# Optimization experiments

Measured on AMD Instinct MI355X. Metric: run time of the kernel, lower is better.

Reference implementation:

```python
import jax, jax.numpy as jnp
import numpy as np

N_NODES = 100000
N_EDGES = 1600000
N_GRAPHS = 512


def gcn_conv(x, src, dst, W, b, num_nodes):
    """PyG GCNConv: add self-loops, sym-normalize, aggregate, add bias."""
    xw = x @ W  # [N, out]
    # degree over destination nodes, +1 for the implicit self-loop
    deg = jax.ops.segment_sum(jnp.ones(src.shape[0], xw.dtype), dst,
                              num_segments=num_nodes) + 1.0
    dinv = jax.lax.rsqrt(deg)  # deg >= 1, safe
    norm = dinv[src] * dinv[dst]  # [E]
    agg = jax.ops.segment_sum(xw[src] * norm[:, None], dst,
                              num_segments=num_nodes)
    # self-loop contribution: dinv[i]^2 * xw[i]
    agg = agg + xw * (dinv * dinv)[:, None]
    return agg + b


def global_mean_pool(x, batch, num_graphs):
    sums = jax.ops.segment_sum(x, batch, num_segments=num_graphs)
    cnts = jax.ops.segment_sum(jnp.ones(x.shape[0], x.dtype), batch,
                               num_segments=num_graphs)
    return sums / jnp.maximum(cnts, 1.0)[:, None]


def setup_inputs() -> dict:
    key = jax.random.key(0)
    ks = jax.random.split(key, 9)
    x = jax.random.normal(ks[0], (N_NODES, 3), dtype=jnp.float32)
    edge_index = jax.random.randint(ks[1], (2, N_EDGES), 0, N_NODES, dtype=jnp.int64)
    batch = jnp.sort(jax.random.randint(ks[2], (N_NODES,), 0, N_GRAPHS, dtype=jnp.int64))
    W1 = jax.random.normal(ks[3], (3, 32), dtype=jnp.float32) * 0.5
    b1 = jax.random.normal(ks[4], (32,), dtype=jnp.float32) * 0.1
    W2 = jax.random.normal(ks[5], (32, 32), dtype=jnp.float32) * 0.2
    b2 = jax.random.normal(ks[6], (32,), dtype=jnp.float32) * 0.1
    Wl = jax.random.normal(ks[7], (32, 2), dtype=jnp.float32) * 0.2
    bl = jax.random.normal(ks[8], (2,), dtype=jnp.float32) * 0.1
    return {"x": x, "edge_index": edge_index, "batch": batch,
            "W1": W1, "b1": b1, "W2": W2, "b2": b2, "Wl": Wl, "bl": bl}


def reference(x, edge_index, batch, W1, b1, W2, b2, Wl, bl):
    src, dst = edge_index[0], edge_index[1]
    h = jax.nn.relu(gcn_conv(x, src, dst, W1, b1, N_NODES))
    h = jax.nn.relu(gcn_conv(h, src, dst, W2, b2, N_NODES))
    g = global_mean_pool(h, batch, N_GRAPHS)  # [G, 32]
    return g @ Wl + bl  # [G, 2]
```

## Files before the change

### kernel.cpp

```cpp
#include <hip/hip_runtime.h>
#include <hip/hip_fp16.h>

#define NN 100000
#define NE 1600000
#define NG 512
#define F  32

#define BSH    8
#define BNODES 256
#define NB     ((NN + BNODES - 1) / BNODES)
#define CAP    5120
#define PCHUNK 4096
#define EPT    8
#define NWGP   ((NE + PCHUNK - 1) / PCHUNK)

__global__ void k_partition(const int* __restrict__ src, const int* __restrict__ dst,
                            int* __restrict__ cursor, int* __restrict__ part) {
    __shared__ int   s_cnt[NB];
    __shared__ int   s_lstart[NB];
    __shared__ int   s_base[NB];
    __shared__ int   wsum[8];
    __shared__ int   lsort[PCHUNK];
    __shared__ short lbkt[PCHUNK];
    int tid = threadIdx.x;
    for (int i = tid; i < NB; i += 512) s_cnt[i] = 0;
    __syncthreads();
    int e0 = blockIdx.x * PCHUNK;
    int e1 = min(e0 + PCHUNK, NE);
    int pk[EPT]; short bk[EPT];
    int m = 0;
#pragma unroll
    for (int k = 0; k < EPT; ++k) {
        int e = e0 + tid + k * 512;
        if (e < e1) {
            int d = dst[e];
            pk[m] = (src[e] << 8) | (d & (BNODES - 1));
            bk[m] = (short)(d >> BSH);
            atomicAdd(&s_cnt[bk[m]], 1);
            ++m;
        }
    }
    __syncthreads();
    int cv = (tid < NB) ? s_cnt[tid] : 0;
    int v = cv;
#pragma unroll
    for (int o = 1; o < 64; o <<= 1) {
        int t = __shfl_up(v, o, 64);
        if ((tid & 63) >= o) v += t;
    }
    if ((tid & 63) == 63) wsum[tid >> 6] = v;
    __syncthreads();
    int add = 0;
    for (int w = 0; w < (tid >> 6); ++w) add += wsum[w];
    int excl = v + add - cv;
    if (tid < NB) {
        s_lstart[tid] = excl;
        if (cv) s_base[tid] = tid * CAP + atomicAdd(&cursor[tid], cv);
        s_cnt[tid] = 0;
    }
    __syncthreads();
    for (int k = 0; k < m; ++k) {
        int b = bk[k];
        int r = s_lstart[b] + atomicAdd(&s_cnt[b], 1);
        lsort[r] = pk[k];
        lbkt[r]  = (short)b;
    }
    __syncthreads();
    int cnt = e1 - e0;
    for (int i = tid; i < cnt; i += 512) {
        int b = lbkt[i];
        part[s_base[b] + (i - s_lstart[b])] = lsort[i];
    }
}

__global__ void k_fill2a(const int* __restrict__ part, const int* __restrict__ cursor,
                         const float* __restrict__ x,
                         int* __restrict__ rowpack, float* __restrict__ dinv,
                         float4* __restrict__ xd) {
    __shared__ int cnt[BNODES];
    __shared__ int wsum[4];
    int b = blockIdx.x, tid = threadIdx.x;
    int node0 = b << BSH;
    int s0 = b * CAP, s1 = s0 + cursor[b];
    cnt[tid] = 0;
    __syncthreads();
    for (int i = s0 + tid; i < s1; i += 256) atomicAdd(&cnt[part[i] & (BNODES - 1)], 1);
    __syncthreads();
    int c = cnt[tid];
    int v = c;
#pragma unroll
    for (int o = 1; o < 64; o <<= 1) {
        int t = __shfl_up(v, o, 64);
        if ((tid & 63) >= o) v += t;
    }
    if ((tid & 63) == 63) wsum[tid >> 6] = v;
    __syncthreads();
    int add = 0;
    for (int w = 0; w < (tid >> 6); ++w) add += wsum[w];
    int excl = v + add - c;
    int n = node0 + tid;
    if (n < NN) {
        rowpack[n] = ((s0 + excl) << 10) | c;
        float d = rsqrtf((float)c + 1.0f);
        dinv[n] = d;
        xd[n] = make_float4(d * x[n * 3 + 0], d * x[n * 3 + 1], d * x[n * 3 + 2], d);
    }
}

__global__ void k_fill2b(const int* __restrict__ part, const int* __restrict__ cursor,
                         const int* __restrict__ rowpack, const float4* __restrict__ xd,
                         const float* __restrict__ W1, const float* __restrict__ b1,
                         int* __restrict__ csr, __half2* __restrict__ g1) {
    __shared__ int lcsr[CAP];
    __shared__ int off[BNODES];
    __shared__ float W1s[3 * F];
    __shared__ float b1s[F];
    int b = blockIdx.x, tid = threadIdx.x;
    int node0 = b << BSH;
    int s0 = b * CAP;
    int cnt = cursor[b];
    if (tid < 3 * F) W1s[tid] = W1[tid];
    if (tid < F) b1s[tid] = b1[tid];
    int n = node0 + tid;
    int pack = (n < NN) ? rowpack[n] : (s0 << 10);
    off[tid] = (pack >> 10) - s0;
    __syncthreads();
    for (int i = tid; i < cnt; i += 256) {
        int p = part[s0 + i];
        int pos = atomicAdd(&off[p & (BNODES - 1)], 1);
        lcsr[pos] = p >> 8;
    }
    __syncthreads();
    for (int i = tid; i < cnt; i += 256) csr[s0 + i] = lcsr[i];
    if (n < NN) {
        int deg = pack & 1023;
        int beg = (pack >> 10) - s0;
        int end = beg + deg;
        float ax = 0.0f, ay = 0.0f, az = 0.0f;
        int e = beg;
        for (; e + 7 < end; e += 8) {
#pragma unroll
            for (int u = 0; u < 8; ++u) {
                float4 v = xd[lcsr[e + u]];
                ax += v.x; ay += v.y; az += v.z;
            }
        }
        for (; e < end; ++e) {
            float4 v = xd[lcsr[e]];
            ax += v.x; ay += v.y; az += v.z;
        }
        float4 sf = xd[n];
        float dn = sf.w;
        float cx = dn * (ax + sf.x), cy = dn * (ay + sf.y), cz = dn * (az + sf.z);
        __half2 tmp[16];
#pragma unroll
        for (int j = 0; j < 16; ++j) {
            int f0 = 2 * j, f1 = 2 * j + 1;
            float v0 = cx * W1s[f0] + cy * W1s[F + f0] + cz * W1s[2 * F + f0] + b1s[f0];
            float v1 = cx * W1s[f1] + cy * W1s[F + f1] + cz * W1s[2 * F + f1] + b1s[f1];
            tmp[j] = __floats2half2_rn(dn * fmaxf(v0, 0.0f), dn * fmaxf(v1, 0.0f));
        }
        uint4* hv = (uint4*)(g1 + (size_t)n * 16);
        const uint4* tv = (const uint4*)tmp;
        hv[0] = tv[0]; hv[1] = tv[1]; hv[2] = tv[2]; hv[3] = tv[3];
    }
}

__global__ void k_gather2p(const int* __restrict__ rowpack, const int* __restrict__ csr,
                           const __half2* __restrict__ g1, const float* __restrict__ dinv,
                           const int* __restrict__ batch,
                           const float* __restrict__ W2, const float* __restrict__ b2,
                           float* __restrict__ gsum) {
    __shared__ float W2s[F * F];
    __shared__ float b2s[F];
    __shared__ float ts[16][F];
    __shared__ float hs[16][F];
    __shared__ int bat[16];
    int tid = threadIdx.x;
    int nb = blockIdx.x * 16;
    for (int i = tid; i < F * F; i += 256) W2s[i] = W2[i];
    if (tid < F) b2s[tid] = b2[tid];
    if (tid < 16) bat[tid] = batch[nb + tid];
    int nl = tid >> 4, j = tid & 15;
    int n = nb + nl;
    {
        int pack = rowpack[n];
        int beg = pack >> 10, end = beg + (pack & 1023);
        float ax = 0.0f, ay = 0.0f;
        int e = beg;
        for (; e + 7 < end; e += 8) {
            int s0 = csr[e],     s1 = csr[e + 1], s2 = csr[e + 2], s3 = csr[e + 3];
            int s4 = csr[e + 4], s5 = csr[e + 5], s6 = csr[e + 6], s7 = csr[e + 7];
            float2 v0 = __half22float2(g1[s0 * 16 + j]);
            float2 v1 = __half22float2(g1[s1 * 16 + j]);
            float2 v2 = __half22float2(g1[s2 * 16 + j]);
            float2 v3 = __half22float2(g1[s3 * 16 + j]);
            float2 v4 = __half22float2(g1[s4 * 16 + j]);
            float2 v5 = __half22float2(g1[s5 * 16 + j]);
            float2 v6 = __half22float2(g1[s6 * 16 + j]);
            float2 v7 = __half22float2(g1[s7 * 16 + j]);
            ax += ((v0.x + v1.x) + (v2.x + v3.x)) + ((v4.x + v5.x) + (v6.x + v7.x));
            ay += ((v0.y + v1.y) + (v2.y + v3.y)) + ((v4.y + v5.y) + (v6.y + v7.y));
        }
        for (; e + 3 < end; e += 4) {
            int s0 = csr[e], s1 = csr[e + 1], s2 = csr[e + 2], s3 = csr[e + 3];
            float2 v0 = __half22float2(g1[s0 * 16 + j]);
            float2 v1 = __half22float2(g1[s1 * 16 + j]);
            float2 v2 = __half22float2(g1[s2 * 16 + j]);
            float2 v3 = __half22float2(g1[s3 * 16 + j]);
            ax += (v0.x + v1.x) + (v2.x + v3.x);
            ay += (v0.y + v1.y) + (v2.y + v3.y);
        }
        for (; e < end; ++e) {
            float2 v = __half22float2(g1[csr[e] * 16 + j]);
            ax += v.x; ay += v.y;
        }
        float dn = dinv[n];
        float2 sf = __half22float2(g1[n * 16 + j]);
        ts[nl][2 * j]     = dn * (ax + sf.x);
        ts[nl][2 * j + 1] = dn * (ay + sf.y);
    }
    __syncthreads();
    {
        int f = tid & 31;
        int nn0 = tid >> 5;
#pragma unroll
        for (int pass = 0; pass < 2; ++pass) {
            int nn = nn0 + pass * 8;
            float acc = b2s[f];
#pragma unroll
            for (int k = 0; k < F; ++k) acc += ts[nn][k] * W2s[k * F + f];
            hs[nn][f] = fmaxf(acc, 0.0f);
        }
    }
    __syncthreads();
    if (tid < F) {
        int g0 = bat[0], gmax = bat[15];
        for (int g = g0; g <= gmax; ++g) {
            float s = 0.0f;
#pragma unroll
            for (int i = 0; i < 16; ++i) if (bat[i] == g) s += hs[i][tid];
            atomicAdd(&gsum[g * F + tid], s);
        }
    }
}

__global__ void k_head(const float* __restrict__ gsum, const int* __restrict__ batch,
                       const float* __restrict__ Wl, const float* __restrict__ bl,
                       float* __restrict__ out) {
    int g = blockIdx.x * blockDim.x + threadIdx.x;
    if (g >= NG) return;
    int lo = 0, hi = NN;
    while (lo < hi) { int m = (lo + hi) >> 1; if (batch[m] < g) lo = m + 1; else hi = m; }
    int s = lo;
    lo = 0; hi = NN;
    while (lo < hi) { int m = (lo + hi) >> 1; if (batch[m] < g + 1) lo = m + 1; else hi = m; }
    float inv = 1.0f / fmaxf((float)(lo - s), 1.0f);
    float a0 = 0.0f, a1 = 0.0f;
#pragma unroll
    for (int k = 0; k < F; ++k) {
        float m = gsum[g * F + k] * inv;
        a0 += m * Wl[k * 2 + 0];
        a1 += m * Wl[k * 2 + 1];
    }
    out[g * 2 + 0] = a0 + bl[0];
    out[g * 2 + 1] = a1 + bl[1];
}

extern "C" void kernel_launch(void* const* d_in, const int* in_sizes, int n_in,
                              void* d_out, int out_size, void* d_ws, size_t ws_size,
                              hipStream_t stream) {
    const float* x     = (const float*)d_in[0];
    const int*   eidx  = (const int*)d_in[1];
    const int*   batch = (const int*)d_in[2];
    const float* W1    = (const float*)d_in[3];
    const float* b1    = (const float*)d_in[4];
    const float* W2    = (const float*)d_in[5];
    const float* b2    = (const float*)d_in[6];
    const float* Wl    = (const float*)d_in[7];
    const float* bl    = (const float*)d_in[8];
    float*       out   = (float*)d_out;

    const int* src = eidx;
    const int* dst = eidx + NE;

    char* base = (char*)d_ws;
    size_t off = 0;
    auto alloc = [&](size_t bytes) {
        void* p = base + off;
        off = (off + bytes + 127) & ~(size_t)127;
        return p;
    };
    int*     cursor  = (int*)alloc(NB * sizeof(int) + (size_t)NG * F * sizeof(float));
    float*   gsum    = (float*)(cursor + NB);
    int*     rowpack = (int*)alloc(NN * sizeof(int));
    int*     part    = (int*)alloc((size_t)NB * CAP * sizeof(int));
    int*     csr     = (int*)alloc((size_t)NB * CAP * sizeof(int));
    float*   dinv    = (float*)alloc(NN * sizeof(float));
    float4*  xd      = (float4*)alloc(NN * sizeof(float4));
    __half2* g1      = (__half2*)alloc((size_t)NN * 16 * sizeof(__half2));

    const int B = 256;
    const int gG16 = NN / 16;

    hipMemsetAsync(cursor, 0, NB * sizeof(int) + (size_t)NG * F * sizeof(float), stream);

    k_partition<<<NWGP, 512, 0, stream>>>(src, dst, cursor, part);
    k_fill2a   <<<NB,   B,   0, stream>>>(part, cursor, x, rowpack, dinv, xd);
    k_fill2b   <<<NB,   B,   0, stream>>>(part, cursor, rowpack, xd, W1, b1, csr, g1);

    k_gather2p<<<gG16, B, 0, stream>>>(rowpack, csr, g1, dinv, batch, W2, b2, gsum);

    k_head<<<(NG + B - 1) / B, B, 0, stream>>>(gsum, batch, Wl, bl, out);
}
```

Measured before the change: 166.4 us.

## Fuse head into gather, use 4 threads per node with 16-byte loads

The layer-2 gather now gives each node 4 threads that each load a uint4 (8 halfs), where it used to give 16 threads that each load a half2. This cuts load instruction count and raises bytes per request. Each block handles 64 nodes. The final linear head is folded into the gather epilogue: per-graph partial sums are projected by Wl, reduced with shuffles, scaled by precomputed inverse counts and atomically added to the output. Inverse counts and bias initialisation move into block 0 of fill2a. This removes the k_head launch and the gsum memset, but adds float-atomic ordering nondeterminism and a serial binary-search tail in one block.

```diff
diff --git a/kernel.cpp b/kernel.cpp
--- a/kernel.cpp
+++ b/kernel.cpp
@@ -74,9 +74,11 @@
 }
 
 __global__ void k_fill2a(const int* __restrict__ part, const int* __restrict__ cursor,
-                         const float* __restrict__ x,
+                         const float* __restrict__ x, const int* __restrict__ batch,
+                         const float* __restrict__ bl,
                          int* __restrict__ rowpack, float* __restrict__ dinv,
-                         float4* __restrict__ xd) {
+                         float4* __restrict__ xd, float* __restrict__ inv_cnt,
+                         float* __restrict__ out) {
     __shared__ int cnt[BNODES];
     __shared__ int wsum[4];
     int b = blockIdx.x, tid = threadIdx.x;
@@ -104,6 +106,20 @@
         float d = rsqrtf((float)c + 1.0f);
         dinv[n] = d;
         xd[n] = make_float4(d * x[n * 3 + 0], d * x[n * 3 + 1], d * x[n * 3 + 2], d);
+    }
+    if (b == 0) {
+        float bl0 = bl[0], bl1 = bl[1];
+#pragma unroll
+        for (int g = tid; g < NG; g += 256) {
+            int lo = 0, hi = NN;
+            while (lo < hi) { int m = (lo + hi) >> 1; if (batch[m] < g) lo = m + 1; else hi = m; }
+            int s = lo;
+            lo = 0; hi = NN;
+            while (lo < hi) { int m = (lo + hi) >> 1; if (batch[m] < g + 1) lo = m + 1; else hi = m; }
+            inv_cnt[g] = 1.0f / fmaxf((float)(lo - s), 1.0f);
+            out[g * 2 + 0] = bl0;
+            out[g * 2 + 1] = bl1;
+        }
     }
 }
 
@@ -170,101 +186,92 @@
                            const __half2* __restrict__ g1, const float* __restrict__ dinv,
                            const int* __restrict__ batch,
                            const float* __restrict__ W2, const float* __restrict__ b2,
-                           float* __restrict__ gsum) {
+                           const float* __restrict__ Wl, const float* __restrict__ inv_cnt,
+                           float* __restrict__ out) {
     __shared__ float W2s[F * F];
     __shared__ float b2s[F];
-    __shared__ float ts[16][F];
-    __shared__ float hs[16][F];
-    __shared__ int bat[16];
+    __shared__ float Wls[F * 2];
+    __shared__ float ts[64][F];
+    __shared__ float hs[64][F];
+    __shared__ int bat[64];
     int tid = threadIdx.x;
-    int nb = blockIdx.x * 16;
+    int nb = blockIdx.x * 64;
     for (int i = tid; i < F * F; i += 256) W2s[i] = W2[i];
     if (tid < F) b2s[tid] = b2[tid];
-    if (tid < 16) bat[tid] = batch[nb + tid];
-    int nl = tid >> 4, j = tid & 15;
-    int n = nb + nl;
-    {
+    if (tid < 2 * F) Wls[tid] = Wl[tid];
+    if (tid < 64) bat[tid] = (nb + tid < NN) ? batch[nb + tid] : -1;
+    int nl = tid >> 2;
+    int j  = tid & 3;
+    int n  = nb + nl;
+    if (n < NN) {
+        const uint4* gp = (const uint4*)g1;
         int pack = rowpack[n];
         int beg = pack >> 10, end = beg + (pack & 1023);
-        float ax = 0.0f, ay = 0.0f;
+        float a0 = 0, a1 = 0, a2 = 0, a3 = 0, a4 = 0, a5 = 0, a6 = 0, a7 = 0;
         int e = beg;
-        for (; e + 7 < end; e += 8) {
-            int s0 = csr[e],     s1 = csr[e + 1], s2 = csr[e + 2], s3 = csr[e + 3];
-            int s4 = csr[e + 4], s5 = csr[e + 5], s6 = csr[e + 6], s7 = csr[e + 7];
-            float2 v0 = __half22float2(g1[s0 * 16 + j]);
-            float2 v1 = __half22float2(g1[s1 * 16 + j]);
-            float2 v2 = __half22float2(g1[s2 * 16 + j]);
-            float2 v3 = __half22float2(g1[s3 * 16 + j]);
-            float2 v4 = __half22float2(g1[s4 * 16 + j]);
-            float2 v5 = __half22float2(g1[s5 * 16 + j]);
-            float2 v6 = __half22float2(g1[s6 * 16 + j]);
-            float2 v7 = __half22float2(g1[s7 * 16 + j]);
-            ax += ((v0.x + v1.x) + (v2.x + v3.x)) + ((v4.x + v5.x) + (v6.x + v7.x));
-            ay += ((v0.y + v1.y) + (v2.y + v3.y)) + ((v4.y + v5.y) + (v6.y + v7.y));
-        }
         for (; e + 3 < end; e += 4) {
             int s0 = csr[e], s1 = csr[e + 1], s2 = csr[e + 2], s3 = csr[e + 3];
-            float2 v0 = __half22float2(g1[s0 * 16 + j]);
-            float2 v1 = __half22float2(g1[s1 * 16 + j]);
-            float2 v2 = __half22float2(g1[s2 * 16 + j]);
-            float2 v3 = __half22float2(g1[s3 * 16 + j]);
-            ax += (v0.x + v1.x) + (v2.x + v3.x);
-            ay += (v0.y + v1.y) + (v2.y + v3.y);
+            uint4 u0 = gp[s0 * 4 + j];
+            uint4 u1 = gp[s1 * 4 + j];
+            uint4 u2 = gp[s2 * 4 + j];
+            uint4 u3 = gp[s3 * 4 + j];
+#define ACC8(u) { \
+            float2 t0 = __half22float2(*(const __half2*)&u.x); \
+            float2 t1 = __half22float2(*(const __half2*)&u.y); \
+            float2 t2 = __half22float2(*(const __half2*)&u.z); \
+            float2 t3 = __half22float2(*(const __half2*)&u.w); \
+            a0 += t0.x; a1 += t0.y; a2 += t1.x; a3 += t1.y; \
+            a4 += t2.x; a5 += t2.y; a6 += t3.x; a7 += t3.y; }
+            ACC8(u0) ACC8(u1) ACC8(u2) ACC8(u3)
         }
         for (; e < end; ++e) {
-            float2 v = __half22float2(g1[csr[e] * 16 + j]);
-            ax += v.x; ay += v.y;
-        }
+            int s = csr[e];
+            uint4 u = gp[s * 4 + j];
+            ACC8(u)
+        }
+        uint4 su = gp[n * 4 + j];
+        ACC8(su)
+#undef ACC8
         float dn = dinv[n];
-        float2 sf = __half22float2(g1[n * 16 + j]);
-        ts[nl][2 * j]     = dn * (ax + sf.x);
-        ts[nl][2 * j + 1] = dn * (ay + sf.y);
+        float* tr = &ts[nl][8 * j];
+        tr[0] = dn * a0; tr[1] = dn * a1; tr[2] = dn * a2; tr[3] = dn * a3;
+        tr[4] = dn * a4; tr[5] = dn * a5; tr[6] = dn * a6; tr[7] = dn * a7;
     }
     __syncthreads();
     {
         int f = tid & 31;
-        int nn0 = tid >> 5;
-#pragma unroll
-        for (int pass = 0; pass < 2; ++pass) {
-            int nn = nn0 + pass * 8;
+        int r = tid >> 5;
+#pragma unroll
+        for (int pass = 0; pass < 8; ++pass) {
+            int nn = r + pass * 8;
             float acc = b2s[f];
 #pragma unroll
             for (int k = 0; k < F; ++k) acc += ts[nn][k] * W2s[k * F + f];
-            hs[nn][f] = fmaxf(acc, 0.0f);
+            hs[nn][f] = (nb + nn < NN) ? fmaxf(acc, 0.0f) : 0.0f;
         }
     }
     __syncthreads();
     if (tid < F) {
-        int g0 = bat[0], gmax = bat[15];
+        int last = min(63, NN - 1 - nb);
+        int g0 = bat[0], gmax = bat[last];
+        float w0 = Wls[2 * tid], w1 = Wls[2 * tid + 1];
         for (int g = g0; g <= gmax; ++g) {
             float s = 0.0f;
 #pragma unroll
-            for (int i = 0; i < 16; ++i) if (bat[i] == g) s += hs[i][tid];
-            atomicAdd(&gsum[g * F + tid], s);
-        }
-    }
-}
-
-__global__ void k_head(const float* __restrict__ gsum, const int* __restrict__ batch,
-                       const float* __restrict__ Wl, const float* __restrict__ bl,
-                       float* __restrict__ out) {
-    int g = blockIdx.x * blockDim.x + threadIdx.x;
-    if (g >= NG) return;
-    int lo = 0, hi = NN;
-    while (lo < hi) { int m = (lo + hi) >> 1; if (batch[m] < g) lo = m + 1; else hi = m; }
-    int s = lo;
-    lo = 0; hi = NN;
-    while (lo < hi) { int m = (lo + hi) >> 1; if (batch[m] < g + 1) lo = m + 1; else hi = m; }
-    float inv = 1.0f / fmaxf((float)(lo - s), 1.0f);
-    float a0 = 0.0f, a1 = 0.0f;
-#pragma unroll
-    for (int k = 0; k < F; ++k) {
-        float m = gsum[g * F + k] * inv;
-        a0 += m * Wl[k * 2 + 0];
-        a1 += m * Wl[k * 2 + 1];
-    }
-    out[g * 2 + 0] = a0 + bl[0];
-    out[g * 2 + 1] = a1 + bl[1];
+            for (int i = 0; i < 64; ++i) if (bat[i] == g) s += hs[i][tid];
+            float p0 = s * w0, p1 = s * w1;
+#pragma unroll
+            for (int o = 16; o >= 1; o >>= 1) {
+                p0 += __shfl_xor(p0, o, 32);
+                p1 += __shfl_xor(p1, o, 32);
+            }
+            if (tid == 0) {
+                float ic = inv_cnt[g];
+                atomicAdd(&out[g * 2 + 0], p0 * ic);
+                atomicAdd(&out[g * 2 + 1], p1 * ic);
+            }
+        }
+    }
 }
 
 extern "C" void kernel_launch(void* const* d_in, const int* in_sizes, int n_in,
@@ -291,8 +298,8 @@
         off = (off + bytes + 127) & ~(size_t)127;
         return p;
     };
-    int*     cursor  = (int*)alloc(NB * sizeof(int) + (size_t)NG * F * sizeof(float));
-    float*   gsum    = (float*)(cursor + NB);
+    int*     cursor  = (int*)alloc(NB * sizeof(int));
+    float*   inv_cnt = (float*)alloc(NG * sizeof(float));
     int*     rowpack = (int*)alloc(NN * sizeof(int));
     int*     part    = (int*)alloc((size_t)NB * CAP * sizeof(int));
     int*     csr     = (int*)alloc((size_t)NB * CAP * sizeof(int));
@@ -301,15 +308,15 @@
     __half2* g1      = (__half2*)alloc((size_t)NN * 16 * sizeof(__half2));
 
     const int B = 256;
-    const int gG16 = NN / 16;
-
-    hipMemsetAsync(cursor, 0, NB * sizeof(int) + (size_t)NG * F * sizeof(float), stream);
+    const int gG64 = (NN + 63) / 64;
+
+    hipMemsetAsync(cursor, 0, NB * sizeof(int), stream);
 
     k_partition<<<NWGP, 512, 0, stream>>>(src, dst, cursor, part);
-    k_fill2a   <<<NB,   B,   0, stream>>>(part, cursor, x, rowpack, dinv, xd);
+    k_fill2a   <<<NB,   B,   0, stream>>>(part, cursor, x, batch, bl,
+                                          rowpack, dinv, xd, inv_cnt, out);
     k_fill2b   <<<NB,   B,   0, stream>>>(part, cursor, rowpack, xd, W1, b1, csr, g1);
 
-    k_gather2p<<<gG16, B, 0, stream>>>(rowpack, csr, g1, dinv, batch, W2, b2, gsum);
-
-    k_head<<<(NG + B - 1) / B, B, 0, stream>>>(gsum, batch, Wl, bl, out);
-}
+    k_gather2p<<<gG64, B, 0, stream>>>(rowpack, csr, g1, dinv, batch, W2, b2,
+                                       Wl, inv_cnt, out);
+}
```

Result: no change. 168.2 us (+1.1%).
